# Optimization experiments

Measured on AMD Instinct MI355X. Metric: run time of the kernel, lower is better.

Reference implementation:

```python
import jax, jax.numpy as jnp
import numpy as np


def setup_inputs() -> dict:
    key = jax.random.key(0)
    k1, k2, k3, k4, k5 = jax.random.split(key, 5)
    B, T, H, E, F = 4, 2048, 2048, 8, 1024
    s_h = 1.0 / np.sqrt(H)
    s_f = 1.0 / np.sqrt(F)
    return {
        "hidden_states": jax.random.normal(k1, (B, T, H), dtype=jnp.float32),
        "W_router": jax.random.normal(k2, (H, E), dtype=jnp.float32) * s_h,
        "W_gate": jax.random.normal(k3, (E, H, F), dtype=jnp.float32) * s_h,
        "W_up": jax.random.normal(k4, (E, H, F), dtype=jnp.float32) * s_h,
        "W_down": jax.random.normal(k5, (E, F, H), dtype=jnp.float32) * s_f,
    }


def reference(hidden_states, W_router, W_gate, W_up, W_down):
    B, T, H = hidden_states.shape
    E = W_router.shape[1]
    x = hidden_states.reshape(-1, H)  # [N, H]
    # ReMoE router: linear -> ReLU, non-negative weights per expert
    weights = jax.nn.relu(x @ W_router)  # [N, E]
    # Per-expert SwiGLU FFN applied to all tokens; zero-weight experts
    # contribute exactly zero, matching the original masked dispatch.
    gate = jnp.einsum('nh,ehf->enf', x, W_gate)  # [E, N, F]
    up = jnp.einsum('nh,ehf->enf', x, W_up)      # [E, N, F]
    hid = jax.nn.silu(gate) * up                 # [E, N, F]
    expert_out = jnp.einsum('enf,efh->enh', hid, W_down)  # [E, N, H]
    out_flat = jnp.einsum('ne,enh->nh', weights, expert_out)  # [N, H]
    out = out_flat.reshape(B, T, H)
    router_weights = weights.reshape(B, T, E)
    return (out, router_weights)
```

## Files before the change

kernel.cpp:

```cpp
#include <hip/hip_runtime.h>
#include <hip/hip_bf16.h>

#define N_TOK 8192
#define HD    2048
#define NE    8
#define FF    1024

using f32x4  = __attribute__((ext_vector_type(4))) float;
using bf16x8 = __attribute__((ext_vector_type(8))) __bf16;

__device__ __forceinline__ unsigned short f2bf(float f) {
  unsigned u = __float_as_uint(f);
  u += 0x7FFFu + ((u >> 16) & 1u);
  return (unsigned short)(u >> 16);
}

__device__ __forceinline__ void gl_lds16(const void* g, void* l) {
  __builtin_amdgcn_global_load_lds((__attribute__((address_space(1))) void*)g,
                                   (__attribute__((address_space(3))) void*)l,
                                   16, 0, 0);
}

__device__ __forceinline__ void stage256(const unsigned short* g, size_t lda, int k0,
                                         char* slotbase, int wv, int sr8, int scol) {
  #pragma unroll
  for (int c = 0; c < 4; ++c) {
    const int grp = c * 8 + wv;
    gl_lds16(g + (size_t)(grp * 8 + sr8) * lda + k0 + scol, slotbase + grp * 1024);
  }
}
__device__ __forceinline__ void stage256i(const unsigned short* const aP[4], int k0,
                                          char* slotbase, int wv) {
  #pragma unroll
  for (int c = 0; c < 4; ++c) {
    const int grp = c * 8 + wv;
    gl_lds16(aP[c] + k0, slotbase + grp * 1024);
  }
}
__device__ __forceinline__ void stage128(const unsigned short* g, size_t lda, int k0,
                                         char* slotbase, int wv, int sr8, int scol) {
  #pragma unroll
  for (int c = 0; c < 2; ++c) {
    const int grp = c * 8 + wv;
    gl_lds16(g + (size_t)(grp * 8 + sr8) * lda + k0 + scol, slotbase + grp * 1024);
  }
}
__device__ __forceinline__ void stage64(const unsigned short* g, size_t lda, int k0,
                                        char* slotbase, int wv, int sr8, int scol) {
  gl_lds16(g + (size_t)(wv * 8 + sr8) * lda + k0 + scol, slotbase + wv * 1024);
}

__global__ void k_tconv(const float* __restrict__ in, unsigned short* __restrict__ out,
                        int R, int C, size_t in_z, size_t out_z, size_t ostride) {
  __shared__ float tile[32][33];
  const int z = blockIdx.z;
  const int c0 = blockIdx.x * 32, r0 = blockIdx.y * 32;
  const int tx = threadIdx.x, ty = threadIdx.y;
  const float* ip = in + (size_t)z * in_z;
  unsigned short* op = out + (size_t)z * out_z;
  #pragma unroll
  for (int i = ty; i < 32; i += 8)
    tile[i][tx] = ip[(size_t)(r0 + i) * C + (c0 + tx)];
  __syncthreads();
  #pragma unroll
  for (int i = ty; i < 32; i += 8)
    op[(size_t)(c0 + i) * ostride + (r0 + tx)] = f2bf(tile[tx][i]);
}

__global__ void k_router(const float* __restrict__ x, const float* __restrict__ Wr,
                         float* __restrict__ w, float* __restrict__ rout,
                         unsigned short* __restrict__ xb) {
  const int lane = threadIdx.x & 63, wv = threadIdx.x >> 6;
  const int n = blockIdx.x * 4 + wv;
  const float* xr = x + (size_t)n * HD + lane * 32;
  unsigned short* xbr = xb + (size_t)n * HD + lane * 32;
  const float* wbase = Wr + (size_t)lane * 32 * NE;
  float acc[8];
  #pragma unroll
  for (int e = 0; e < 8; ++e) acc[e] = 0.f;
  #pragma unroll
  for (int kk = 0; kk < 32; kk += 4) {
    float4 xv = *reinterpret_cast<const float4*>(xr + kk);
    ushort4 o;
    o.x = f2bf(xv.x); o.y = f2bf(xv.y); o.z = f2bf(xv.z); o.w = f2bf(xv.w);
    *reinterpret_cast<ushort4*>(xbr + kk) = o;
    #pragma unroll
    for (int t = 0; t < 4; ++t) {
      const float* wrow = wbase + (kk + t) * 8;
      float4 w0 = *reinterpret_cast<const float4*>(wrow);
      float4 w1 = *reinterpret_cast<const float4*>(wrow + 4);
      float xs = (t == 0) ? xv.x : (t == 1) ? xv.y : (t == 2) ? xv.z : xv.w;
      acc[0] += xs * w0.x; acc[1] += xs * w0.y; acc[2] += xs * w0.z; acc[3] += xs * w0.w;
      acc[4] += xs * w1.x; acc[5] += xs * w1.y; acc[6] += xs * w1.z; acc[7] += xs * w1.w;
    }
  }
  #pragma unroll
  for (int off = 32; off; off >>= 1) {
    #pragma unroll
    for (int e = 0; e < 8; ++e) acc[e] += __shfl_down(acc[e], off);
  }
  if (lane == 0) {
    #pragma unroll
    for (int e = 0; e < 8; ++e) {
      float v = acc[e] > 0.f ? acc[e] : 0.f;
      w[n * 8 + e] = v;
      rout[n * 8 + e] = v;
    }
  }
}

__global__ void k_compact(const float* __restrict__ w, int* __restrict__ idx,
                          int* __restrict__ cnt) {
  const int e = blockIdx.x;
  __shared__ int base;
  __shared__ int scan[4];
  if (threadIdx.x == 0) base = 0;
  __syncthreads();
  const int lane = threadIdx.x & 63, wvi = threadIdx.x >> 6;
  for (int c0 = 0; c0 < N_TOK; c0 += 256) {
    const int n = c0 + threadIdx.x;
    const bool act = w[n * 8 + e] > 0.f;
    unsigned long long m = __ballot(act);
    const int pre  = __popcll(m & ((1ull << lane) - 1ull));
    if (lane == 0) scan[wvi] = __popcll(m);
    __syncthreads();
    int woff = 0;
    #pragma unroll
    for (int i = 0; i < 4; ++i) if (i < wvi) woff += scan[i];
    const int tot = scan[0] + scan[1] + scan[2] + scan[3];
    if (act) idx[e * N_TOK + base + woff + pre] = n;
    __syncthreads();
    if (threadIdx.x == 0) base += tot;
    __syncthreads();
  }
  const int M = base;
  if (threadIdx.x == 0) cnt[e] = M;
  const int Mpad = (M + 255) & ~255;
  for (int i = M + threadIdx.x; i < Mpad; i += 256) idx[e * N_TOK + i] = 0;
}

#define G1_PHASE(cpK) do {                                                       \
    const char* Ab_ = As + sA * 32768 + (wr * 64) * 128 + rb;                    \
    const char* Bg_ = Bgs + sBr * 8192 + (wc * 32) * 128 + rb;                   \
    const char* Bu_ = Bus + sBr * 8192 + (wc * 32) * 128 + rb;                   \
    bf16x8 av_[4], bg_[2], bu_[2];                                               \
    _Pragma("unroll")                                                            \
    for (int i = 0; i < 4; ++i) av_[i] = *(const bf16x8*)(Ab_ + i * 2048 + (cpK)); \
    _Pragma("unroll")                                                            \
    for (int j = 0; j < 2; ++j) {                                                \
      bg_[j] = *(const bf16x8*)(Bg_ + j * 2048 + (cpK));                         \
      bu_[j] = *(const bf16x8*)(Bu_ + j * 2048 + (cpK));                         \
    }                                                                            \
    __builtin_amdgcn_s_setprio(1);                                               \
    _Pragma("unroll")                                                            \
    for (int i = 0; i < 4; ++i) {                                                \
      _Pragma("unroll")                                                          \
      for (int j = 0; j < 2; ++j) {                                              \
        ag[i][j] = __builtin_amdgcn_mfma_f32_16x16x32_bf16(av_[i], bg_[j], ag[i][j], 0,0,0); \
        au[i][j] = __builtin_amdgcn_mfma_f32_16x16x32_bf16(av_[i], bu_[j], au[i][j], 0,0,0); \
      }                                                                          \
    }                                                                            \
    __builtin_amdgcn_s_setprio(0);                                               \
  } while (0)

__global__ void __launch_bounds__(512, 2) k_gemm1(
    const unsigned short* __restrict__ xb,
    const unsigned short* __restrict__ Wg,
    const unsigned short* __restrict__ Wu,
    const float* __restrict__ w,
    const int* __restrict__ idx,
    const int* __restrict__ cnt,
    unsigned short* __restrict__ A2,
    int e0, int k2g, int nwg) {
  extern __shared__ char lds[];
  char* As  = lds;
  char* Bgs = lds + 98304;
  char* Bus = lds + 114688;
  const int tid = threadIdx.x;
  const int l = tid & 63, wv = tid >> 6;

  const int h = blockIdx.x;
  const int chunk = nwg >> 3;
  const int L = (h & 7) * chunk + (h >> 3);
  const int eloc = L >> 9;
  const int e = e0 + eloc;
  const int idxq = L & 511;
  const int sub = idxq >> 5;
  const int f = ((sub & 3) << 2) | ((idxq >> 3) & 3);
  const int y = ((sub >> 2) << 3) | (idxq & 7);
  const int bm = y << 8;
  const int bf = f << 6;
  const int wr = wv >> 1, wc = wv & 1;

  const int Me = cnt[e];
  if (bm >= Me) return;
  const int* idxe = idx + e * N_TOK;

  const unsigned short* gBg = Wg + ((size_t)e * FF + bf) * HD;
  const unsigned short* gBu = Wu + ((size_t)e * FF + bf) * HD;

  const int sr8  = l >> 3;
  const int scol = ((l & 7) ^ sr8) << 3;
  const int fr  = l & 15;
  const int rb  = fr << 7;
  const int kc  = (l >> 4) << 4;
  const int swz = (l & 7) << 4;
  const int cp0 = kc ^ swz;
  const int cp1 = (64 + kc) ^ swz;

  const unsigned short* aP[4];
  #pragma unroll
  for (int c = 0; c < 4; ++c)
    aP[c] = xb + (size_t)idxe[bm + (c * 8 + wv) * 8 + sr8] * HD + scol;

  f32x4 ag[4][2], au[4][2];
  const f32x4 zero = {0.f, 0.f, 0.f, 0.f};
  #pragma unroll
  for (int i = 0; i < 4; ++i) {
    #pragma unroll
    for (int j = 0; j < 2; ++j) { ag[i][j] = zero; au[i][j] = zero; }
  }

  stage256i(aP, 0, As, wv);
  stage64(gBg, HD, 0, Bgs, wv, sr8, scol);
  stage64(gBu, HD, 0, Bus, wv, sr8, scol);
  stage256i(aP, 64, As + 32768, wv);
  asm volatile("s_waitcnt vmcnt(4)" ::: "memory");
  __builtin_amdgcn_s_barrier();
  __builtin_amdgcn_sched_barrier(0);

  const int NT = HD / 64;
  int sA = 0;
  for (int t = 0; t < NT; ++t) {
    const int tB = (t + 1 < NT) ? t + 1 : NT - 1;
    const int tA = (t + 2 < NT) ? t + 2 : NT - 1;
    const int sBw = (t + 1) & 1;
    const int sBr = t & 1;
    const int sAw = (sA >= 1) ? sA - 1 : 2;
    stage64(gBg, HD, tB * 64, Bgs + sBw * 8192, wv, sr8, scol);
    stage64(gBu, HD, tB * 64, Bus + sBw * 8192, wv, sr8, scol);
    G1_PHASE(cp0);
    stage256i(aP, tA * 64, As + sAw * 32768, wv);
    G1_PHASE(cp1);
    asm volatile("s_waitcnt vmcnt(4)" ::: "memory");
    __builtin_amdgcn_s_barrier();
    __builtin_amdgcn_sched_barrier(0);
    sA = (sA == 2) ? 0 : sA + 1;
  }

  const int orow = (l >> 4) << 2;
  #pragma unroll
  for (int am = 0; am < 4; ++am) {
    #pragma unroll
    for (int rr = 0; rr < 4; ++rr) {
      const int cm = bm + wr * 64 + am * 16 + orow + rr;
      const int n = idxe[cm];
      const float wn = w[n * 8 + e];
      size_t obase = (size_t)n * k2g + (size_t)eloc * FF + bf + wc * 32 + fr;
      #pragma unroll
      for (int j = 0; j < 2; ++j) {
        const float g = ag[am][j][rr];
        const float u = au[am][j][rr];
        const float s = g / (1.f + __expf(-g));
        A2[obase + j * 16] = f2bf(s * u * wn);
      }
    }
  }
}

#define G2_PHASE(cpK) do {                                                       \
    const char* Ab_ = As + sA * 32768 + (wr * 64) * 128 + rb;                    \
    const char* Bb_ = Bs + sBr * 16384 + (wc * 64) * 128 + rb;                   \
    bf16x8 av_[4], bv_[4];                                                       \
    _Pragma("unroll")                                                            \
    for (int i = 0; i < 4; ++i) av_[i] = *(const bf16x8*)(Ab_ + i * 2048 + (cpK)); \
    _Pragma("unroll")                                                            \
    for (int j = 0; j < 4; ++j) bv_[j] = *(const bf16x8*)(Bb_ + j * 2048 + (cpK)); \
    __builtin_amdgcn_s_setprio(1);                                               \
    _Pragma("unroll")                                                            \
    for (int i = 0; i < 4; ++i) {                                                \
      _Pragma("unroll")                                                          \
      for (int j = 0; j < 4; ++j)                                                \
        acc[i][j] = __builtin_amdgcn_mfma_f32_16x16x32_bf16(av_[i], bv_[j], acc[i][j], 0,0,0); \
    }                                                                            \
    __builtin_amdgcn_s_setprio(0);                                               \
  } while (0)

__global__ void __launch_bounds__(512, 2) k_gemm2(
    const unsigned short* __restrict__ A2,
    const unsigned short* __restrict__ Wd,
    float* __restrict__ out,
    int k2g, int accum) {
  extern __shared__ char lds[];
  char* As = lds;
  char* Bs = lds + 98304;
  const int tid = threadIdx.x;
  const int l = tid & 63, wv = tid >> 6;

  const int h = blockIdx.x;
  const int L = (h & 7) * 64 + (h >> 3);
  const int y = L >> 4;
  const int x = L & 15;
  const int bm = y << 8;
  const int bn = x << 7;
  const int wr = wv >> 1, wc = wv & 1;

  const unsigned short* gA = A2 + (size_t)bm * k2g;
  const unsigned short* gB = Wd + (size_t)bn * (NE * FF);

  const int sr8  = l >> 3;
  const int scol = ((l & 7) ^ sr8) << 3;
  const int fr  = l & 15;
  const int rb  = fr << 7;
  const int kc  = (l >> 4) << 4;
  const int swz = (l & 7) << 4;
  const int cp0 = kc ^ swz;
  const int cp1 = (64 + kc) ^ swz;

  f32x4 acc[4][4];
  const f32x4 zero = {0.f, 0.f, 0.f, 0.f};
  #pragma unroll
  for (int i = 0; i < 4; ++i) {
    #pragma unroll
    for (int j = 0; j < 4; ++j) acc[i][j] = zero;
  }

  stage256(gA, k2g, 0, As, wv, sr8, scol);
  stage128(gB, NE * FF, 0, Bs, wv, sr8, scol);
  stage256(gA, k2g, 64, As + 32768, wv, sr8, scol);
  asm volatile("s_waitcnt vmcnt(4)" ::: "memory");
  __builtin_amdgcn_s_barrier();
  __builtin_amdgcn_sched_barrier(0);

  const int NT = k2g / 64;
  int sA = 0;
  for (int t = 0; t < NT; ++t) {
    const int tB = (t + 1 < NT) ? t + 1 : NT - 1;
    const int tA = (t + 2 < NT) ? t + 2 : NT - 1;
    const int sBw = (t + 1) & 1;
    const int sBr = t & 1;
    const int sAw = (sA >= 1) ? sA - 1 : 2;
    stage128(gB, NE * FF, tB * 64, Bs + sBw * 16384, wv, sr8, scol);
    G2_PHASE(cp0);
    stage256(gA, k2g, tA * 64, As + sAw * 32768, wv, sr8, scol);
    G2_PHASE(cp1);
    asm volatile("s_waitcnt vmcnt(4)" ::: "memory");
    __builtin_amdgcn_s_barrier();
    __builtin_amdgcn_sched_barrier(0);
    sA = (sA == 2) ? 0 : sA + 1;
  }

  const int orow = (l >> 4) << 2;
  #pragma unroll
  for (int am = 0; am < 4; ++am) {
    #pragma unroll
    for (int rr = 0; rr < 4; ++rr) {
      const int n = bm + wr * 64 + am * 16 + orow + rr;
      float* op = out + (size_t)n * HD + bn + wc * 64 + fr;
      #pragma unroll
      for (int j = 0; j < 4; ++j) {
        const float v = acc[am][j][rr];
        op[j * 16] = accum ? (op[j * 16] + v) : v;
      }
    }
  }
}

extern "C" void kernel_launch(void* const* d_in, const int* in_sizes, int n_in,
                              void* d_out, int out_size, void* d_ws, size_t ws_size,
                              hipStream_t stream) {
  (void)in_sizes; (void)out_size;
  if (n_in < 5) return;
  const float* x  = (const float*)d_in[0];
  const float* Wr = (const float*)d_in[1];
  const float* Wg = (const float*)d_in[2];
  const float* Wu = (const float*)d_in[3];
  const float* Wd = (const float*)d_in[4];
  float* out  = (float*)d_out;
  float* rout = out + (size_t)N_TOK * HD;

  hipFuncSetAttribute((const void*)k_gemm1, hipFuncAttributeMaxDynamicSharedMemorySize, 131072);
  hipFuncSetAttribute((const void*)k_gemm2, hipFuncAttributeMaxDynamicSharedMemorySize, 131072);

  char* ws = (char*)d_ws;
  const size_t SZ_XB = (size_t)N_TOK * HD * 2;
  const size_t SZ_W  = (size_t)NE * HD * FF * 2;
  unsigned short* xb    = (unsigned short*)(ws);
  unsigned short* Wg_bt = (unsigned short*)(ws + SZ_XB);
  unsigned short* Wu_bt = (unsigned short*)(ws + SZ_XB + SZ_W);
  unsigned short* Wd_bt = (unsigned short*)(ws + SZ_XB + 2 * SZ_W);
  float*          wbuf  = (float*)(ws + SZ_XB + 3 * SZ_W);
  size_t off = SZ_XB + 3 * SZ_W + (size_t)N_TOK * NE * 4;
  int* idxbuf = (int*)(ws + off);  off += (size_t)NE * N_TOK * 4;
  int* cntbuf = (int*)(ws + off);  off += 256;
  const size_t fixed = off;
  unsigned short* A2 = (unsigned short*)(ws + fixed);

  const size_t perE = (size_t)N_TOK * FF * 2;
  int G = 8;
  while (G > 1 && fixed + (size_t)G * perE > ws_size) G >>= 1;

  dim3 tb(32, 8);
  k_tconv<<<dim3(FF / 32, HD / 32, NE), tb, 0, stream>>>(
      Wg, Wg_bt, HD, FF, (size_t)HD * FF, (size_t)FF * HD, (size_t)HD);
  k_tconv<<<dim3(FF / 32, HD / 32, NE), tb, 0, stream>>>(
      Wu, Wu_bt, HD, FF, (size_t)HD * FF, (size_t)FF * HD, (size_t)HD);
  k_tconv<<<dim3(HD / 32, FF / 32, NE), tb, 0, stream>>>(
      Wd, Wd_bt, FF, HD, (size_t)FF * HD, (size_t)FF, (size_t)(NE * FF));

  k_router<<<N_TOK / 4, 256, 0, stream>>>(x, Wr, wbuf, rout, xb);

  k_compact<<<NE, 256, 0, stream>>>(wbuf, idxbuf, cntbuf);

  const int k2g = G * FF;
  for (int e0 = 0; e0 < NE; e0 += G) {
    hipMemsetAsync(A2, 0, (size_t)G * perE, stream);
    const int nwg1 = 512 * G;
    k_gemm1<<<nwg1, 512, 131072, stream>>>(xb, Wg_bt, Wu_bt, wbuf, idxbuf, cntbuf,
                                           A2, e0, k2g, nwg1);
    k_gemm2<<<512, 512, 131072, stream>>>(A2, Wd_bt + (size_t)e0 * FF, out, k2g, e0 != 0);
  }
}
```

Before: 738.2 us.

## Enlarge GEMM tiles and switch to double-buffered single-stage prefetch

GEMM1 output tile widens from 64 to 128 F columns per workgroup (256 tokens x 128 for both gate and up), and GEMM2 tile grows from 256x128 to 256x256. With larger B tiles, the triple-buffered A with two-ahead prefetch is replaced by plain double buffering with one-tile lookahead and a full vmcnt(0) wait each step. The aim is to raise arithmetic intensity and cut redundant loads of the token rows and weights. The cost is double the accumulator registers (64 f32x4 per thread in GEMM1, 32 in GEMM2) at launch_bounds(512,2), which risks spills or lower occupancy, plus less latency hiding because every step waits for all loads to finish.

```diff
diff --git a/kernel.cpp b/kernel.cpp
--- a/kernel.cpp
+++ b/kernel.cpp
@@ -44,10 +44,6 @@
     const int grp = c * 8 + wv;
     gl_lds16(g + (size_t)(grp * 8 + sr8) * lda + k0 + scol, slotbase + grp * 1024);
   }
-}
-__device__ __forceinline__ void stage64(const unsigned short* g, size_t lda, int k0,
-                                        char* slotbase, int wv, int sr8, int scol) {
-  gl_lds16(g + (size_t)(wv * 8 + sr8) * lda + k0 + scol, slotbase + wv * 1024);
 }
 
 __global__ void k_tconv(const float* __restrict__ in, unsigned short* __restrict__ out,
@@ -140,14 +136,14 @@
 }
 
 #define G1_PHASE(cpK) do {                                                       \
-    const char* Ab_ = As + sA * 32768 + (wr * 64) * 128 + rb;                    \
-    const char* Bg_ = Bgs + sBr * 8192 + (wc * 32) * 128 + rb;                   \
-    const char* Bu_ = Bus + sBr * 8192 + (wc * 32) * 128 + rb;                   \
-    bf16x8 av_[4], bg_[2], bu_[2];                                               \
+    const char* Ab_ = As + rs * 32768 + (wr * 64) * 128 + rb;                    \
+    const char* Bg_ = Bgs + rs * 16384 + (wc * 64) * 128 + rb;                   \
+    const char* Bu_ = Bus + rs * 16384 + (wc * 64) * 128 + rb;                   \
+    bf16x8 av_[4], bg_[4], bu_[4];                                               \
     _Pragma("unroll")                                                            \
     for (int i = 0; i < 4; ++i) av_[i] = *(const bf16x8*)(Ab_ + i * 2048 + (cpK)); \
     _Pragma("unroll")                                                            \
-    for (int j = 0; j < 2; ++j) {                                                \
+    for (int j = 0; j < 4; ++j) {                                                \
       bg_[j] = *(const bf16x8*)(Bg_ + j * 2048 + (cpK));                         \
       bu_[j] = *(const bf16x8*)(Bu_ + j * 2048 + (cpK));                         \
     }                                                                            \
@@ -155,7 +151,7 @@
     _Pragma("unroll")                                                            \
     for (int i = 0; i < 4; ++i) {                                                \
       _Pragma("unroll")                                                          \
-      for (int j = 0; j < 2; ++j) {                                              \
+      for (int j = 0; j < 4; ++j) {                                              \
         ag[i][j] = __builtin_amdgcn_mfma_f32_16x16x32_bf16(av_[i], bg_[j], ag[i][j], 0,0,0); \
         au[i][j] = __builtin_amdgcn_mfma_f32_16x16x32_bf16(av_[i], bu_[j], au[i][j], 0,0,0); \
       }                                                                          \
@@ -174,22 +170,22 @@
     int e0, int k2g, int nwg) {
   extern __shared__ char lds[];
   char* As  = lds;
-  char* Bgs = lds + 98304;
-  char* Bus = lds + 114688;
+  char* Bgs = lds + 65536;
+  char* Bus = lds + 98304;
   const int tid = threadIdx.x;
   const int l = tid & 63, wv = tid >> 6;
 
   const int h = blockIdx.x;
   const int chunk = nwg >> 3;
   const int L = (h & 7) * chunk + (h >> 3);
-  const int eloc = L >> 9;
+  const int eloc = L >> 8;
   const int e = e0 + eloc;
-  const int idxq = L & 511;
+  const int idxq = L & 255;
   const int sub = idxq >> 5;
-  const int f = ((sub & 3) << 2) | ((idxq >> 3) & 3);
-  const int y = ((sub >> 2) << 3) | (idxq & 7);
+  const int f = ((sub & 1) << 2) | ((idxq >> 3) & 3);
+  const int y = ((sub >> 1) << 3) | (idxq & 7);
   const int bm = y << 8;
-  const int bf = f << 6;
+  const int bf = f << 7;
   const int wr = wv >> 1, wc = wv & 1;
 
   const int Me = cnt[e];
@@ -213,39 +209,34 @@
   for (int c = 0; c < 4; ++c)
     aP[c] = xb + (size_t)idxe[bm + (c * 8 + wv) * 8 + sr8] * HD + scol;
 
-  f32x4 ag[4][2], au[4][2];
+  f32x4 ag[4][4], au[4][4];
   const f32x4 zero = {0.f, 0.f, 0.f, 0.f};
   #pragma unroll
   for (int i = 0; i < 4; ++i) {
     #pragma unroll
-    for (int j = 0; j < 2; ++j) { ag[i][j] = zero; au[i][j] = zero; }
+    for (int j = 0; j < 4; ++j) { ag[i][j] = zero; au[i][j] = zero; }
   }
 
   stage256i(aP, 0, As, wv);
-  stage64(gBg, HD, 0, Bgs, wv, sr8, scol);
-  stage64(gBu, HD, 0, Bus, wv, sr8, scol);
-  stage256i(aP, 64, As + 32768, wv);
-  asm volatile("s_waitcnt vmcnt(4)" ::: "memory");
+  stage128(gBg, HD, 0, Bgs, wv, sr8, scol);
+  stage128(gBu, HD, 0, Bus, wv, sr8, scol);
+  asm volatile("s_waitcnt vmcnt(0)" ::: "memory");
   __builtin_amdgcn_s_barrier();
   __builtin_amdgcn_sched_barrier(0);
 
   const int NT = HD / 64;
-  int sA = 0;
   for (int t = 0; t < NT; ++t) {
-    const int tB = (t + 1 < NT) ? t + 1 : NT - 1;
-    const int tA = (t + 2 < NT) ? t + 2 : NT - 1;
-    const int sBw = (t + 1) & 1;
-    const int sBr = t & 1;
-    const int sAw = (sA >= 1) ? sA - 1 : 2;
-    stage64(gBg, HD, tB * 64, Bgs + sBw * 8192, wv, sr8, scol);
-    stage64(gBu, HD, tB * 64, Bus + sBw * 8192, wv, sr8, scol);
+    const int tn = (t + 1 < NT) ? t + 1 : NT - 1;
+    const int sw = (t + 1) & 1;
+    const int rs = t & 1;
+    stage128(gBg, HD, tn * 64, Bgs + sw * 16384, wv, sr8, scol);
+    stage128(gBu, HD, tn * 64, Bus + sw * 16384, wv, sr8, scol);
     G1_PHASE(cp0);
-    stage256i(aP, tA * 64, As + sAw * 32768, wv);
+    stage256i(aP, tn * 64, As + sw * 32768, wv);
     G1_PHASE(cp1);
-    asm volatile("s_waitcnt vmcnt(4)" ::: "memory");
+    asm volatile("s_waitcnt vmcnt(0)" ::: "memory");
     __builtin_amdgcn_s_barrier();
     __builtin_amdgcn_sched_barrier(0);
-    sA = (sA == 2) ? 0 : sA + 1;
   }
 
   const int orow = (l >> 4) << 2;
@@ -256,9 +247,9 @@
       const int cm = bm + wr * 64 + am * 16 + orow + rr;
       const int n = idxe[cm];
       const float wn = w[n * 8 + e];
-      size_t obase = (size_t)n * k2g + (size_t)eloc * FF + bf + wc * 32 + fr;
+      size_t obase = (size_t)n * k2g + (size_t)eloc * FF + bf + wc * 64 + fr;
       #pragma unroll
-      for (int j = 0; j < 2; ++j) {
+      for (int j = 0; j < 4; ++j) {
         const float g = ag[am][j][rr];
         const float u = au[am][j][rr];
         const float s = g / (1.f + __expf(-g));
@@ -269,16 +260,16 @@
 }
 
 #define G2_PHASE(cpK) do {                                                       \
-    const char* Ab_ = As + sA * 32768 + (wr * 64) * 128 + rb;                    \
-    const char* Bb_ = Bs + sBr * 16384 + (wc * 64) * 128 + rb;                   \
-    bf16x8 av_[4], bv_[4];                                                       \
-    _Pragma("unroll")                                                            \
-    for (int i = 0; i < 4; ++i) av_[i] = *(const bf16x8*)(Ab_ + i * 2048 + (cpK)); \
+    const char* Ab_ = As + rs * 32768 + (wr * 128) * 128 + rb;                   \
+    const char* Bb_ = Bs + rs * 32768 + (wc * 64) * 128 + rb;                    \
+    bf16x8 av_[8], bv_[4];                                                       \
+    _Pragma("unroll")                                                            \
+    for (int i = 0; i < 8; ++i) av_[i] = *(const bf16x8*)(Ab_ + i * 2048 + (cpK)); \
     _Pragma("unroll")                                                            \
     for (int j = 0; j < 4; ++j) bv_[j] = *(const bf16x8*)(Bb_ + j * 2048 + (cpK)); \
     __builtin_amdgcn_s_setprio(1);                                               \
     _Pragma("unroll")                                                            \
-    for (int i = 0; i < 4; ++i) {                                                \
+    for (int i = 0; i < 8; ++i) {                                                \
       _Pragma("unroll")                                                          \
       for (int j = 0; j < 4; ++j)                                                \
         acc[i][j] = __builtin_amdgcn_mfma_f32_16x16x32_bf16(av_[i], bv_[j], acc[i][j], 0,0,0); \
@@ -293,17 +284,17 @@
     int k2g, int accum) {
   extern __shared__ char lds[];
   char* As = lds;
-  char* Bs = lds + 98304;
+  char* Bs = lds + 65536;
   const int tid = threadIdx.x;
   const int l = tid & 63, wv = tid >> 6;
 
   const int h = blockIdx.x;
-  const int L = (h & 7) * 64 + (h >> 3);
-  const int y = L >> 4;
-  const int x = L & 15;
+  const int L = (h & 7) * 32 + (h >> 3);
+  const int y = L >> 3;
+  const int x = L & 7;
   const int bm = y << 8;
-  const int bn = x << 7;
-  const int wr = wv >> 1, wc = wv & 1;
+  const int bn = x << 8;
+  const int wr = wv >> 2, wc = wv & 3;
 
   const unsigned short* gA = A2 + (size_t)bm * k2g;
   const unsigned short* gB = Wd + (size_t)bn * (NE * FF);
@@ -317,45 +308,40 @@
   const int cp0 = kc ^ swz;
   const int cp1 = (64 + kc) ^ swz;
 
-  f32x4 acc[4][4];
+  f32x4 acc[8][4];
   const f32x4 zero = {0.f, 0.f, 0.f, 0.f};
   #pragma unroll
-  for (int i = 0; i < 4; ++i) {
+  for (int i = 0; i < 8; ++i) {
     #pragma unroll
     for (int j = 0; j < 4; ++j) acc[i][j] = zero;
   }
 
   stage256(gA, k2g, 0, As, wv, sr8, scol);
-  stage128(gB, NE * FF, 0, Bs, wv, sr8, scol);
-  stage256(gA, k2g, 64, As + 32768, wv, sr8, scol);
-  asm volatile("s_waitcnt vmcnt(4)" ::: "memory");
+  stage256(gB, NE * FF, 0, Bs, wv, sr8, scol);
+  asm volatile("s_waitcnt vmcnt(0)" ::: "memory");
   __builtin_amdgcn_s_barrier();
   __builtin_amdgcn_sched_barrier(0);
 
   const int NT = k2g / 64;
-  int sA = 0;
   for (int t = 0; t < NT; ++t) {
-    const int tB = (t + 1 < NT) ? t + 1 : NT - 1;
-    const int tA = (t + 2 < NT) ? t + 2 : NT - 1;
-    const int sBw = (t + 1) & 1;
-    const int sBr = t & 1;
-    const int sAw = (sA >= 1) ? sA - 1 : 2;
-    stage128(gB, NE * FF, tB * 64, Bs + sBw * 16384, wv, sr8, scol);
+    const int tn = (t + 1 < NT) ? t + 1 : NT - 1;
+    const int sw = (t + 1) & 1;
+    const int rs = t & 1;
+    stage256(gB, NE * FF, tn * 64, Bs + sw * 32768, wv, sr8, scol);
     G2_PHASE(cp0);
-    stage256(gA, k2g, tA * 64, As + sAw * 32768, wv, sr8, scol);
+    stage256(gA, k2g, tn * 64, As + sw * 32768, wv, sr8, scol);
     G2_PHASE(cp1);
-    asm volatile("s_waitcnt vmcnt(4)" ::: "memory");
+    asm volatile("s_waitcnt vmcnt(0)" ::: "memory");
     __builtin_amdgcn_s_barrier();
     __builtin_amdgcn_sched_barrier(0);
-    sA = (sA == 2) ? 0 : sA + 1;
   }
 
   const int orow = (l >> 4) << 2;
   #pragma unroll
-  for (int am = 0; am < 4; ++am) {
+  for (int am = 0; am < 8; ++am) {
     #pragma unroll
     for (int rr = 0; rr < 4; ++rr) {
-      const int n = bm + wr * 64 + am * 16 + orow + rr;
+      const int n = bm + wr * 128 + am * 16 + orow + rr;
       float* op = out + (size_t)n * HD + bn + wc * 64 + fr;
       #pragma unroll
       for (int j = 0; j < 4; ++j) {
@@ -415,9 +401,10 @@
   const int k2g = G * FF;
   for (int e0 = 0; e0 < NE; e0 += G) {
     hipMemsetAsync(A2, 0, (size_t)G * perE, stream);
-    const int nwg1 = 512 * G;
+    const int nwg1 = 256 * G;
     k_gemm1<<<nwg1, 512, 131072, stream>>>(xb, Wg_bt, Wu_bt, wbuf, idxbuf, cntbuf,
                                            A2, e0, k2g, nwg1);
-    k_gemm2<<<512, 512, 131072, stream>>>(A2, Wd_bt + (size_t)e0 * FF, out, k2g, e0 != 0);
-  }
-}
+    k_gemm2<<<(N_TOK / 256) * (HD / 256), 512, 131072, stream>>>(
+        A2, Wd_bt + (size_t)e0 * FF, out, k2g, e0 != 0);
+  }
+}
```

Result: faster. 690.4 us (-6.5%).
